# Performance work log

Hardware: AMD Instinct MI355X
Metric: run time of the kernel (lower is better)

The kernel has to match this reference:

```python
import jax, jax.numpy as jnp
import numpy as np

ROWS, COLS = 4096, 2048
NUM_BITS = 4
NUM_LEVELS = 2 ** NUM_BITS  # 16
FIXED_T = 100.0
EPS = 1e-06


def setup_inputs() -> dict:
    key = jax.random.key(0)
    kw, = jax.random.split(key, 1)
    weight = jax.random.normal(kw, (ROWS, COLS), dtype=jnp.float32)
    col_min = weight.min(axis=0)
    col_max = weight.max(axis=0)
    pad = 0.01 * (col_max - col_min)
    w_min = col_min - pad  # [COLS]
    w_max = col_max + pad  # [COLS]
    return {"weight": weight, "w_min": w_min, "w_max": w_max}


def reference(weight, w_min, w_max):
    # Torch clamps against the *detached scalar* of the other bound -> stop_gradient
    w_min_c = jnp.minimum(w_min, jax.lax.stop_gradient(w_max) - EPS)          # [C]
    w_max_c = jnp.maximum(w_max, jax.lax.stop_gradient(w_min_c) + EPS)        # [C]
    rng = w_max_c - w_min_c                                                   # [C]

    q_levels = jnp.linspace(0.0, 1.0, NUM_LEVELS, dtype=weight.dtype)         # [L]

    w_norm = (weight - w_min_c[None, :]) / (rng[None, :] + EPS)               # [R, C]
    dists = -jnp.abs(w_norm[:, :, None] - q_levels[None, None, :])            # [R, C, L]
    soft_probs = jax.nn.softmax(dists * FIXED_T, axis=-1)                     # [R, C, L]

    w_q = jnp.einsum("rcl,l->rc", soft_probs, q_levels)                       # [R, C]
    w_dequant = w_q * rng[None, :] + w_min_c[None, :]                         # [R, C]

    bin_mass = soft_probs.sum(axis=0)                                         # [C, L]
    bin_probs = bin_mass / (bin_mass.sum(axis=-1, keepdims=True) + EPS)       # [C, L]
    entropy_per_col = -(bin_probs * jnp.log(bin_probs + EPS)).sum(axis=-1)    # [C]
    total_entropy = entropy_per_col.sum()

    return (w_dequant, total_entropy)
```

## Files before the change

kernel.cpp:

```cpp
#include <hip/hip_runtime.h>

#define ROWS 4096
#define COLS 2048
#define NLEV 16
#define TEMP 100.0f
#define EPS  1e-6f
#define LOG2E 1.4426950408889634f
#define RGEO 1.2726338e-3f
#define C2P  1.2710160e-3f
#define C1PP (1.0f + 2.0f * C2P)

#define TPB 256
#define RPB 32
#define RBLKS (ROWS / RPB)
#define UNROLL 8

typedef _Float16 half8_t __attribute__((ext_vector_type(8)));
typedef _Float16 half2_t __attribute__((ext_vector_type(2)));


__global__ __launch_bounds__(TPB) void quant_main_kernel(
    const float* __restrict__ weight,
    const float* __restrict__ w_min,
    const float* __restrict__ w_max,
    float* __restrict__ dequant,
    _Float16* __restrict__ partial,
    float* __restrict__ out_ent)
{
    const int t  = threadIdx.x;
    const int c  = blockIdx.x * TPB + t;
    const int r0 = blockIdx.y * RPB;

    if (blockIdx.x == 0 && blockIdx.y == 0 && t == 0) out_ent[0] = 0.0f;

    const float wmin = w_min[c];
    const float wmax = w_max[c];
    const float mn   = fminf(wmin, wmax - EPS);
    const float mx   = fmaxf(wmax, mn + EPS);
    const float rng  = mx - mn;
    const float inv_rng = __builtin_amdgcn_rcpf(rng + EPS);

    const float S     = (TEMP / 15.0f) * LOG2E;
    const float s15   = 15.0f * inv_rng;
    const float b15   = -mn * s15;
    const float rng15 = rng * (1.0f / 15.0f);

    half2_t G2[8];
#pragma unroll
    for (int i = 0; i < 8; ++i) G2[i] = (half2_t){(_Float16)0, (_Float16)0};

    half2_t A2[8];
#pragma unroll
    for (int i = 0; i < 8; ++i) {
        A2[i] = (half2_t){(_Float16)(1 - 2 * i), (_Float16)(-2 * i)};
        asm("" : "+v"(A2[i]));
    }

    const float* __restrict__ wp = weight  + (size_t)r0 * COLS + c;
    float* __restrict__       dq = dequant + (size_t)r0 * COLS + c;

    for (int r = 0; r < RPB; r += UNROLL) {
        float w[UNROLL];
#pragma unroll
        for (int j = 0; j < UNROLL; ++j)
            w[j] = wp[(size_t)(r + j) * COLS];

#pragma unroll
        for (int j = 0; j < UNROLL; ++j) {
            const float y  = fmaf(w[j], s15, b15);
            float kf = floorf(y);
            kf = fminf(fmaxf(kf, 0.0f), 14.0f);

            const float q  = fmaf(y - kf, 2.0f * S, -S);
            const float e  = __builtin_amdgcn_exp2f(q);
            const float uv = e * __builtin_amdgcn_rcpf(1.0f + e);

            __builtin_nontemporal_store(
                fmaf(fmaf(uv, C1PP, kf - C2P), rng15, mn),
                &dq[(size_t)(r + j) * COLS]);

            const float Pr = kf + uv;
            const _Float16 Ph = (_Float16)Pr;
            const half2_t P2 = {Ph, Ph};
#pragma unroll
            for (int i = 0; i < 8; ++i) {
                half2_t d;
                asm("v_pk_add_f16 %0, %1, %2 clamp"
                    : "=v"(d) : "v"(P2), "v"(A2[i]));
                G2[i] += d;
            }
        }
    }

    float g[17];
#pragma unroll
    for (int l = 0; l < NLEV; ++l) g[l] = (float)G2[l >> 1][l & 1];
    g[16] = 0.0f;

    half8_t v0, v1;
#pragma unroll
    for (int l = 0; l < NLEV; ++l) {
        const float bin = g[l] - g[l + 1];
        if (l < 8) v0[l] = (_Float16)bin; else v1[l - 8] = (_Float16)bin;
    }
    half8_t* pp = (half8_t*)(partial + ((size_t)blockIdx.y * COLS + c) * NLEV);
    pp[0] = v0;
    pp[1] = v1;
}

__global__ __launch_bounds__(256) void reduce_entropy_kernel(
    const _Float16* __restrict__ partial,
    float* __restrict__ out_ent)
{
    __shared__ float red[256];
    const int i = blockIdx.x * 256 + threadIdx.x;
    const half2_t* p2 = (const half2_t*)partial;

    float m0 = 0.0f, m1 = 0.0f;
#pragma unroll 16
    for (int rb = 0; rb < RBLKS; ++rb) {
        const half2_t v = p2[(size_t)rb * (COLS * NLEV / 2) + i];
        m0 += (float)v[0];
        m1 += (float)v[1];
    }

    float tot = m0 + m1;
    tot += __shfl_xor(tot, 1);
    tot += __shfl_xor(tot, 2);
    tot += __shfl_xor(tot, 4);
    const float inv = __builtin_amdgcn_rcpf(tot + EPS);

    const float p0 = m0 * inv;
    const float p1 = m1 * inv;
    float ent = -(p0 * __logf(p0 + EPS) + p1 * __logf(p1 + EPS));

    red[threadIdx.x] = ent;
    __syncthreads();
#pragma unroll
    for (int off = 128; off > 0; off >>= 1) {
        if (threadIdx.x < off) red[threadIdx.x] += red[threadIdx.x + off];
        __syncthreads();
    }
    if (threadIdx.x == 0) atomicAdd(out_ent, red[0]);
}

extern "C" void kernel_launch(void* const* d_in, const int* in_sizes, int n_in,
                              void* d_out, int out_size, void* d_ws, size_t ws_size,
                              hipStream_t stream)
{
    const float* weight = (const float*)d_in[0];
    const float* w_min  = (const float*)d_in[1];
    const float* w_max  = (const float*)d_in[2];

    float* out     = (float*)d_out;
    float* dequant = out;
    float* out_ent = out + (size_t)ROWS * COLS;
    _Float16* partial = (_Float16*)d_ws;

    quant_main_kernel<<<dim3(COLS / TPB, RBLKS), TPB, 0, stream>>>(
        weight, w_min, w_max, dequant, partial, out_ent);

    reduce_entropy_kernel<<<(COLS * NLEV / 2) / 256, 256, 0, stream>>>(
        partial, out_ent);
}
```

Measured before the change: 94.29 us.

## Double-buffer weight loads, double rows per block, accumulate bins in fp32

```diff
diff --git a/kernel.cpp b/kernel.cpp
--- a/kernel.cpp
+++ b/kernel.cpp
@@ -11,9 +11,10 @@
 #define C1PP (1.0f + 2.0f * C2P)
 
 #define TPB 256
-#define RPB 32
+#define RPB 64
 #define RBLKS (ROWS / RPB)
 #define UNROLL 8
+#define RTPB 128
 
 typedef _Float16 half8_t __attribute__((ext_vector_type(8)));
 typedef _Float16 half2_t __attribute__((ext_vector_type(2)));
@@ -45,9 +46,9 @@
     const float b15   = -mn * s15;
     const float rng15 = rng * (1.0f / 15.0f);
 
-    half2_t G2[8];
+    float gacc[NLEV];
 #pragma unroll
-    for (int i = 0; i < 8; ++i) G2[i] = (half2_t){(_Float16)0, (_Float16)0};
+    for (int l = 0; l < NLEV; ++l) gacc[l] = 0.0f;
 
     half2_t A2[8];
 #pragma unroll
@@ -59,11 +60,24 @@
     const float* __restrict__ wp = weight  + (size_t)r0 * COLS + c;
     float* __restrict__       dq = dequant + (size_t)r0 * COLS + c;
 
+    float w[UNROLL];
+#pragma unroll
+    for (int j = 0; j < UNROLL; ++j)
+        w[j] = __builtin_nontemporal_load(&wp[(size_t)j * COLS]);
+
     for (int r = 0; r < RPB; r += UNROLL) {
-        float w[UNROLL];
+        float wn[UNROLL];
+        const bool more = (r + UNROLL) < RPB;
+        if (more) {
 #pragma unroll
-        for (int j = 0; j < UNROLL; ++j)
-            w[j] = wp[(size_t)(r + j) * COLS];
+            for (int j = 0; j < UNROLL; ++j)
+                wn[j] = __builtin_nontemporal_load(
+                    &wp[(size_t)(r + UNROLL + j) * COLS]);
+        }
+
+        half2_t G2[8];
+#pragma unroll
+        for (int i = 0; i < 8; ++i) G2[i] = (half2_t){(_Float16)0, (_Float16)0};
 
 #pragma unroll
         for (int j = 0; j < UNROLL; ++j) {
@@ -90,12 +104,20 @@
                 G2[i] += d;
             }
         }
+
+#pragma unroll
+        for (int l = 0; l < NLEV; ++l) gacc[l] += (float)G2[l >> 1][l & 1];
+
+        if (more) {
+#pragma unroll
+            for (int j = 0; j < UNROLL; ++j) w[j] = wn[j];
+        }
     }
 
-    float g[17];
+    float g[NLEV + 1];
 #pragma unroll
-    for (int l = 0; l < NLEV; ++l) g[l] = (float)G2[l >> 1][l & 1];
-    g[16] = 0.0f;
+    for (int l = 0; l < NLEV; ++l) g[l] = gacc[l];
+    g[NLEV] = 0.0f;
 
     half8_t v0, v1;
 #pragma unroll
@@ -108,12 +130,12 @@
     pp[1] = v1;
 }
 
-__global__ __launch_bounds__(256) void reduce_entropy_kernel(
+__global__ __launch_bounds__(RTPB) void reduce_entropy_kernel(
     const _Float16* __restrict__ partial,
     float* __restrict__ out_ent)
 {
-    __shared__ float red[256];
-    const int i = blockIdx.x * 256 + threadIdx.x;
+    __shared__ float red[RTPB];
+    const int i = blockIdx.x * RTPB + threadIdx.x;
     const half2_t* p2 = (const half2_t*)partial;
 
     float m0 = 0.0f, m1 = 0.0f;
@@ -137,7 +159,7 @@
     red[threadIdx.x] = ent;
     __syncthreads();
 #pragma unroll
-    for (int off = 128; off > 0; off >>= 1) {
+    for (int off = RTPB / 2; off > 0; off >>= 1) {
         if (threadIdx.x < off) red[threadIdx.x] += red[threadIdx.x + off];
         __syncthreads();
     }
@@ -160,6 +182,6 @@
     quant_main_kernel<<<dim3(COLS / TPB, RBLKS), TPB, 0, stream>>>(
         weight, w_min, w_max, dequant, partial, out_ent);
 
-    reduce_entropy_kernel<<<(COLS * NLEV / 2) / 256, 256, 0, stream>>>(
+    reduce_entropy_kernel<<<(COLS * NLEV / 2) / RTPB, RTPB, 0, stream>>>(
         partial, out_ent);
 }
```

New measurement: 101.9 us. 8.0% more time.
